# Kernel optimization log

Hardware: AMD Instinct MI355X
Metric: run time of the kernel (lower is better)

The kernel has to match this reference:

```python
import jax, jax.numpy as jnp
import numpy as np

HORIZON_K = 20
EPS = 1e-8


def _unfold_gather(x, time_idx, k):
    # Emulates zero-pad + tensor.unfold(1, k, 1).permute(3,0,1,2) + index_select(2, time_idx)
    # x: [N, T-1, C] -> [k, N, S, C] where out[ki, n, s] = x_padded[n, time_idx[s] + ki]
    N, Tm1, C = x.shape
    xp = jnp.concatenate([x, jnp.zeros((N, k, C), x.dtype)], axis=1)
    gidx = time_idx[None, :] + jnp.arange(k)[:, None]  # [k, S]
    return jnp.transpose(xp[:, gidx, :], (1, 0, 2, 3))  # [k, N, S, C]


def _gru_rollout(x_seq, h0, W_ih, W_hh, b_ih, b_hh):
    # x_seq: [k, B, A]; h0: [B, H]; torch GRU gate order: r, z, n
    H = h0.shape[-1]
    def step(h, x):
        gi = x @ W_ih.T + b_ih          # [B, 3H]
        gh = h @ W_hh.T + b_hh          # [B, 3H]
        r = jax.nn.sigmoid(gi[:, :H] + gh[:, :H])
        z = jax.nn.sigmoid(gi[:, H:2 * H] + gh[:, H:2 * H])
        n = jnp.tanh(gi[:, 2 * H:] + r * gh[:, 2 * H:])
        hn = (1.0 - z) * n + z * h
        return hn, hn
    _, hs = jax.lax.scan(step, h0, x_seq)
    return hs  # [k, B, H]


def _mlp(x, W1, b1, W2, b2, W3, b3):
    x = jax.nn.relu(x @ W1 + b1)
    x = jax.nn.relu(x @ W2 + b2)
    return x @ W3 + b3


def _l2norm(x):
    n = jnp.linalg.norm(x, axis=-1, keepdims=True)
    return x / jnp.maximum(n, EPS)


def setup_inputs() -> dict:
    key = jax.random.key(0)
    ks = jax.random.split(key, 16)
    N, T, H, A, M = 1024, 128, 256, 18, 512
    g = lambda k, sh, s: jax.random.normal(k, sh, jnp.float32) * s
    return {
        "actions": jax.random.randint(ks[0], (N, T), 0, A),
        "dones": jnp.zeros((N, T), jnp.float32),
        "b_t": g(ks[1], (N * T, H), 1.0),
        "z_t": g(ks[2], (N * T, H), 1.0),
        "time_subsample": jax.random.randint(ks[3], (6,), 0, T - 1),
        "unroll_subsample": jax.random.randint(ks[4], (2,), 0, HORIZON_K),
        "W_ih": g(ks[5], (3 * H, A), 0.05), "W_hh": g(ks[6], (3 * H, H), 0.05),
        "b_ih": g(ks[7], (3 * H,), 0.05), "b_hh": g(ks[8], (3 * H,), 0.05),
        "W1": g(ks[9], (H, M), 0.05), "b1": g(ks[10], (M,), 0.05),
        "W2": g(ks[11], (M, M), 0.05), "b2": g(ks[12], (M,), 0.05),
        "W3": g(ks[13], (M, H), 0.05), "b3": g(ks[14], (H,), 0.05),
    }


def reference(actions, dones, b_t, z_t, time_subsample, unroll_subsample,
              W_ih, W_hh, b_ih, b_hh, W1, b1, W2, b2, W3, b3):
    N, T = actions.shape
    H = b_t.shape[-1]
    A = W_ih.shape[1]
    k = HORIZON_K

    # mask (dones fixed to all-zero -> max_k == horizon_k)
    not_dones = (1.0 - dones).reshape(N, T, 1)
    nd_unf = _unfold_gather(not_dones[:, :-1], time_subsample, k)        # [k,N,S,1]
    fmask = jnp.cumprod(nd_unf, axis=0).reshape(k, -1, 1)                # [k,N*S,1]
    fmask = (fmask[unroll_subsample] > 0).astype(jnp.float32)            # [F,B,1]

    # unfolded one-hot actions
    onehot = jax.nn.one_hot(actions, A, dtype=jnp.float32)               # [N,T,A]
    act_unf = _unfold_gather(onehot[:, :-1], time_subsample, k)          # [k,N,S,A]
    act_unf = act_unf.reshape(k, -1, A)                                  # [k,B,A]

    # GRU initial states from core outputs at subsampled times
    c = b_t.reshape(N, T, H)[:, :-1][:, time_subsample]                  # [N,S,H]
    h0 = c.reshape(-1, H)                                                # [B,H]

    # 20-step open-loop GRU rollout
    h_pred = _gru_rollout(act_unf, h0, W_ih, W_hh, b_ih, b_hh)           # [k,B,H]
    h_pred = h_pred[unroll_subsample]                                    # [F,B,H]

    final_pred = _mlp(h_pred, W1, b1, W2, b2, W3, b3)                    # [F,B,H]
    norm = jnp.linalg.norm(final_pred, axis=2)
    reg = 0.02 * jnp.square(norm - 1.0)                                  # [F,B]
    final_pred = _l2norm(final_pred)

    # targets (no grad): unfolded future encodings, normalized
    z = jax.lax.stop_gradient(z_t).reshape(N, T, -1)
    tgt = _unfold_gather(z[:, 1:], time_subsample, k)                    # [k,N,S,C]
    tgt = tgt[unroll_subsample].reshape(len(unroll_subsample), -1, z.shape[-1])
    tgt = _l2norm(tgt)                                                   # [F,B,C]

    loss = jnp.square(final_pred - tgt)                                  # [F,B,C]
    loss = loss.mean(-1, keepdims=True)                                  # [F,B,1]
    loss = jnp.sum(loss * fmask) / jnp.maximum(jnp.sum(fmask), 1.0)
    return loss + reg.mean()
```

## Files before the change

### kernel.cpp

```cpp
#include <hip/hip_runtime.h>
#include <hip/hip_bf16.h>
#include <math.h>

#define NN 1024
#define TT 128
#define SS 6
#define FF 2
#define HH 256
#define AA 18
#define MM 512
#define KH 20
#define BB (NN*SS)
#define RR (FF*BB)
#define LOSS_BLOCKS 1024

#define SCL_RZ (-1.44269504089f)
#define SCL_N  (-2.88539008178f)
#define TBL_STRIDE 784

typedef __bf16 bf16x8 __attribute__((ext_vector_type(8)));
typedef float f32x4 __attribute__((ext_vector_type(4)));

__device__ __forceinline__ f32x4 mfma16(bf16x8 a, bf16x8 b, f32x4 c) {
    return __builtin_amdgcn_mfma_f32_16x16x32_bf16(a, b, c, 0, 0, 0);
}
__device__ __forceinline__ unsigned short f2b(float f) {
    return __builtin_bit_cast(unsigned short, __float2bfloat16(f));
}
__device__ __forceinline__ float rcp_f(float x)  { return __builtin_amdgcn_rcpf(x); }
__device__ __forceinline__ float exp2_f(float x) { return __builtin_amdgcn_exp2f(x); }

#define OFF_ACT   0UL
#define OFF_HPRED 491520UL
#define OFF_PRED  6782976UL
#define OFF_WHH   19365888UL
#define OFF_W1T   19759104UL
#define OFF_W2T   20021248UL
#define OFF_W3T   20545536UL
#define OFF_TBL   20807680UL
#define OFF_PART  20867264UL

__global__ void k_prep(const float* __restrict__ Whh, const float* __restrict__ W1,
                       const float* __restrict__ W2, const float* __restrict__ W3,
                       const float* __restrict__ Wih, const float* __restrict__ bih,
                       const float* __restrict__ bhh,
                       const int* __restrict__ actions, const int* __restrict__ ts,
                       unsigned short* whh_s, unsigned short* w1t, unsigned short* w2t,
                       unsigned short* w3t, float* tbl, int* act) {
    int idx = blockIdx.x * 256 + threadIdx.x;
    if (idx < 196608) {
        int wrow = idx >> 8;
        float scl = (wrow < 512) ? SCL_RZ : SCL_N;
        whh_s[idx] = f2b(Whh[idx] * scl);
        return;
    }
    idx -= 196608;
    if (idx < 131072) { int m = idx >> 8, k = idx & 255; w1t[idx] = f2b(W1[k * MM + m]); return; }
    idx -= 131072;
    if (idx < 262144) { int m = idx >> 9, k = idx & 511; w2t[idx] = f2b(W2[k * MM + m]); return; }
    idx -= 262144;
    if (idx < 131072) { int c = idx >> 9, k = idx & 511; w3t[idx] = f2b(W3[k * HH + c]); return; }
    idx -= 131072;
    if (idx < 19 * TBL_STRIDE) {
        int a = idx / TBL_STRIDE, rem = idx - a * TBL_STRIDE;
        float v = 0.f;
        if (rem < 768) {
            int g = rem >> 8;
            float scl = (g < 2) ? SCL_RZ : SCL_N;
            float w = (a < AA) ? Wih[rem * AA + a] : 0.f;
            v = scl * (w + bih[rem] + ((g < 2) ? bhh[rem] : 0.f));
        }
        tbl[idx] = v;
        return;
    }
    idx -= 19 * TBL_STRIDE;
    {
        int b = idx / KH, k = idx - b * KH;
        int n = b / SS, s = b - n * SS;
        int tt = ts[s] + k;
        act[idx] = (tt < TT - 1) ? actions[n * TT + tt] : AA;
    }
}

__global__ void __launch_bounds__(512, 2)
k_gru_all(const unsigned short* __restrict__ whh_s, const float* __restrict__ tblg,
          const float* __restrict__ bhh, const int* __restrict__ actg,
          const int* __restrict__ us, const int* __restrict__ ts,
          const float* __restrict__ b_t, unsigned short* __restrict__ hpred) {
    __shared__ float tbl[19 * TBL_STRIDE];
    __shared__ int act_l[16][KH];
    __shared__ unsigned short htile[16][264];

    int tid = threadIdx.x, wave = tid >> 6, lane = tid & 63;
    int l15 = lane & 15, grp = lane >> 4, lk8 = grp << 3, r4 = grp << 2;
    int rb = blockIdx.x * 16;
    int u0 = us[0], u1 = us[1];
    int kmax = u0 > u1 ? u0 : u1;

    for (int i = tid; i < 19 * TBL_STRIDE / 4; i += 512)
        reinterpret_cast<float4*>(tbl)[i] = reinterpret_cast<const float4*>(tblg)[i];
    if (tid < 16 * KH) {
        int r = tid / KH, k = tid - r * KH;
        act_l[r][k] = actg[(rb + r) * KH + k];
    }

    bf16x8 wr[6][8];
#pragma unroll
    for (int ct = 0; ct < 6; ++ct) {
        int wrow = (ct >> 1) * 256 + wave * 32 + (ct & 1) * 16 + l15;
        const unsigned short* base = &whh_s[(size_t)wrow * HH];
#pragma unroll
        for (int kk = 0; kk < 8; ++kk)
            wr[ct][kk] = *reinterpret_cast<const bf16x8*>(&base[kk * 32 + lk8]);
    }

    float hm[2][4];
#pragma unroll
    for (int cj = 0; cj < 2; ++cj)
#pragma unroll
        for (int reg = 0; reg < 4; ++reg) {
            int b = rb + r4 + reg;
            int n = b / SS, s = b - n * SS;
            hm[cj][reg] = b_t[(size_t)(n * TT + ts[s]) * HH + wave * 32 + cj * 16 + l15];
        }
    float bhn[2];
#pragma unroll
    for (int cj = 0; cj < 2; ++cj) bhn[cj] = SCL_N * bhh[512 + wave * 32 + cj * 16 + l15];

    {
        int row = tid >> 5, c8 = (tid & 31) << 3;
        int b = rb + row;
        int n = b / SS, s = b - n * SS;
        const float* src = &b_t[(size_t)(n * TT + ts[s]) * HH + c8];
        uint4 pk;
        pk.x = f2b(src[0]) | ((unsigned)f2b(src[1]) << 16);
        pk.y = f2b(src[2]) | ((unsigned)f2b(src[3]) << 16);
        pk.z = f2b(src[4]) | ((unsigned)f2b(src[5]) << 16);
        pk.w = f2b(src[6]) | ((unsigned)f2b(src[7]) << 16);
        *reinterpret_cast<uint4*>(&htile[row][c8]) = pk;
    }
    __syncthreads();

    for (int ki = 0; ki <= kmax; ++ki) {
        f32x4 aR[2] = {}, aZ[2] = {}, aN[2] = {};
#pragma unroll
        for (int kk = 0; kk < 8; ++kk) {
            bf16x8 ah = *reinterpret_cast<const bf16x8*>(&htile[l15][kk * 32 + lk8]);
            aR[0] = mfma16(ah, wr[0][kk], aR[0]);
            aR[1] = mfma16(ah, wr[1][kk], aR[1]);
            aZ[0] = mfma16(ah, wr[2][kk], aZ[0]);
            aZ[1] = mfma16(ah, wr[3][kk], aZ[1]);
            aN[0] = mfma16(ah, wr[4][kk], aN[0]);
            aN[1] = mfma16(ah, wr[5][kk], aN[1]);
        }
        __syncthreads();

#pragma unroll
        for (int cj = 0; cj < 2; ++cj) {
            int j2 = wave * 32 + cj * 16 + l15;
            float bhnv = bhn[cj];
#pragma unroll
            for (int reg = 0; reg < 4; ++reg) {
                int row = r4 + reg;
                const float* tb = &tbl[act_l[row][ki] * TBL_STRIDE];
                float r = rcp_f(1.f + exp2_f(aR[cj][reg] + tb[j2]));
                float z = rcp_f(1.f + exp2_f(aZ[cj][reg] + tb[256 + j2]));
                float ghn = aN[cj][reg] + bhnv;
                float nv = 2.f * rcp_f(1.f + exp2_f(tb[512 + j2] + r * ghn)) - 1.f;
                float h = hm[cj][reg];
                float hn2 = nv + z * (h - nv);
                hm[cj][reg] = hn2;
                unsigned short hbv = f2b(hn2);
                htile[row][j2] = hbv;
                if (ki == u0) hpred[(size_t)(rb + row) * HH + j2] = hbv;
                if (ki == u1) hpred[(size_t)(BB + rb + row) * HH + j2] = hbv;
            }
        }
        __syncthreads();
    }
}

__device__ __forceinline__ int xsw(int row, int chunk) {
    return (row << 9) + ((chunk ^ (row & 7)) << 3);
}

__global__ void __launch_bounds__(512, 2)
k_mlp_all(const unsigned short* __restrict__ hpred, const unsigned short* __restrict__ w1t,
          const unsigned short* __restrict__ w2t, const unsigned short* __restrict__ w3t,
          const float* __restrict__ b1, const float* __restrict__ b2,
          const float* __restrict__ b3, float* __restrict__ pred) {
    __shared__ unsigned short xs[48 * 512];
    int tid = threadIdx.x, wave = tid >> 6, lane = tid & 63;
    int l15 = lane & 15, grp = lane >> 4, lk8 = grp << 3, r4 = grp << 2;
    int rb = blockIdx.x * 48;

    {
        f32x4 acc[3][4] = {};
        for (int kk = 0; kk < 8; ++kk) {
            int k0 = kk * 32 + lk8;
            bf16x8 av[3];
#pragma unroll
            for (int rt = 0; rt < 3; ++rt)
                av[rt] = *reinterpret_cast<const bf16x8*>(&hpred[(size_t)(rb + rt * 16 + l15) * HH + k0]);
#pragma unroll
            for (int ct = 0; ct < 4; ++ct) {
                int col = wave * 64 + ct * 16 + l15;
                bf16x8 bv = *reinterpret_cast<const bf16x8*>(&w1t[(size_t)col * HH + k0]);
#pragma unroll
                for (int rt = 0; rt < 3; ++rt) acc[rt][ct] = mfma16(av[rt], bv, acc[rt][ct]);
            }
        }
#pragma unroll
        for (int ct = 0; ct < 4; ++ct) {
            int col = wave * 64 + ct * 16 + l15;
            float bb = b1[col];
#pragma unroll
            for (int rt = 0; rt < 3; ++rt)
#pragma unroll
                for (int reg = 0; reg < 4; ++reg) {
                    int row = rt * 16 + r4 + reg;
                    xs[xsw(row, col >> 3) + (col & 7)] = f2b(fmaxf(acc[rt][ct][reg] + bb, 0.f));
                }
        }
    }
    __syncthreads();

    {
        f32x4 acc[3][4] = {};
        for (int kk = 0; kk < 16; ++kk) {
            bf16x8 av[3];
#pragma unroll
            for (int rt = 0; rt < 3; ++rt)
                av[rt] = *reinterpret_cast<const bf16x8*>(&xs[xsw(rt * 16 + l15, kk * 4 + grp)]);
#pragma unroll
            for (int ct = 0; ct < 4; ++ct) {
                int col = wave * 64 + ct * 16 + l15;
                bf16x8 bv = *reinterpret_cast<const bf16x8*>(&w2t[(size_t)col * MM + kk * 32 + lk8]);
#pragma unroll
                for (int rt = 0; rt < 3; ++rt) acc[rt][ct] = mfma16(av[rt], bv, acc[rt][ct]);
            }
        }
        __syncthreads();
#pragma unroll
        for (int ct = 0; ct < 4; ++ct) {
            int col = wave * 64 + ct * 16 + l15;
            float bb = b2[col];
#pragma unroll
            for (int rt = 0; rt < 3; ++rt)
#pragma unroll
                for (int reg = 0; reg < 4; ++reg) {
                    int row = rt * 16 + r4 + reg;
                    xs[xsw(row, col >> 3) + (col & 7)] = f2b(fmaxf(acc[rt][ct][reg] + bb, 0.f));
                }
        }
    }
    __syncthreads();

    {
        f32x4 acc[3][2] = {};
        for (int kk = 0; kk < 16; ++kk) {
            bf16x8 av[3];
#pragma unroll
            for (int rt = 0; rt < 3; ++rt)
                av[rt] = *reinterpret_cast<const bf16x8*>(&xs[xsw(rt * 16 + l15, kk * 4 + grp)]);
#pragma unroll
            for (int ct = 0; ct < 2; ++ct) {
                int col = wave * 32 + ct * 16 + l15;
                bf16x8 bv = *reinterpret_cast<const bf16x8*>(&w3t[(size_t)col * MM + kk * 32 + lk8]);
#pragma unroll
                for (int rt = 0; rt < 3; ++rt) acc[rt][ct] = mfma16(av[rt], bv, acc[rt][ct]);
            }
        }
#pragma unroll
        for (int ct = 0; ct < 2; ++ct) {
            int col = wave * 32 + ct * 16 + l15;
            float bb = b3[col];
#pragma unroll
            for (int rt = 0; rt < 3; ++rt)
#pragma unroll
                for (int reg = 0; reg < 4; ++reg) {
                    int row = rt * 16 + r4 + reg;
                    pred[(size_t)(rb + row) * HH + col] = acc[rt][ct][reg] + bb;
                }
        }
    }
}

__global__ void k_loss(const float* __restrict__ pred, const float* __restrict__ z_t,
                       const float* __restrict__ dones, const int* __restrict__ ts,
                       const int* __restrict__ us, float* part) {
    int wave = threadIdx.x >> 6, lane = threadIdx.x & 63;
    float mse_l = 0.f;
    float cnt_l = 0.f, reg_l = 0.f;

    for (int i = 0; i < 3; ++i) {
        int row = blockIdx.x * 12 + wave * 3 + i;
        int f = row / BB, b = row - f * BB;
        int n = b / SS, s = b - n * SS;
        int t = ts[s], u = us[f];

        const float* pr = pred + (size_t)row * HH;
        float pv[4], ssq = 0.f;
#pragma unroll
        for (int q = 0; q < 4; ++q) { pv[q] = pr[lane + 64 * q]; ssq += pv[q] * pv[q]; }
        for (int o = 32; o; o >>= 1) ssq += __shfl_xor(ssq, o);
        float norm = sqrtf(ssq);
        if (lane == 0) { float d = norm - 1.f; reg_l += 0.02f * d * d; }

        bool valid = (t + u) < (TT - 1);
        if (valid) {
            float m = 1.f;
            for (int jj = 0; jj <= u; ++jj) m *= (1.f - dones[n * TT + t + jj]);
            valid = (m > 0.f);
        }
        if (!valid) continue;

        const float* zr = z_t + (size_t)(n * TT + 1 + t + u) * HH;
        float zv[4], zsq = 0.f;
#pragma unroll
        for (int q = 0; q < 4; ++q) { zv[q] = zr[lane + 64 * q]; zsq += zv[q] * zv[q]; }
        for (int o = 32; o; o >>= 1) zsq += __shfl_xor(zsq, o);
        float tn = sqrtf(zsq);

        float ip = 1.f / fmaxf(norm, 1e-8f);
        float it = 1.f / fmaxf(tn, 1e-8f);
        float e = 0.f;
#pragma unroll
        for (int q = 0; q < 4; ++q) { float d = pv[q] * ip - zv[q] * it; e += d * d; }
        mse_l += e * (1.f / HH);
        if (lane == 0) cnt_l += 1.f;
    }

    for (int o = 32; o; o >>= 1) mse_l += __shfl_xor(mse_l, o);

    __shared__ float sm[4][3];
    if (lane == 0) { sm[wave][0] = mse_l; sm[wave][1] = cnt_l; sm[wave][2] = reg_l; }
    __syncthreads();
    if (threadIdx.x == 0) {
        float s0 = 0.f, s1 = 0.f, s2 = 0.f;
        for (int w = 0; w < 4; ++w) { s0 += sm[w][0]; s1 += sm[w][1]; s2 += sm[w][2]; }
        part[blockIdx.x * 3 + 0] = s0;
        part[blockIdx.x * 3 + 1] = s1;
        part[blockIdx.x * 3 + 2] = s2;
    }
}

__global__ void k_final(const float* __restrict__ part, float* out) {
    int tid = threadIdx.x, wave = tid >> 6, lane = tid & 63;
    float s0 = 0.f, s1 = 0.f, s2 = 0.f;
    for (int i = tid; i < LOSS_BLOCKS; i += 256) {
        s0 += part[i * 3 + 0];
        s1 += part[i * 3 + 1];
        s2 += part[i * 3 + 2];
    }
    for (int o = 32; o; o >>= 1) {
        s0 += __shfl_xor(s0, o);
        s1 += __shfl_xor(s1, o);
        s2 += __shfl_xor(s2, o);
    }
    __shared__ float sm[4][3];
    if (lane == 0) { sm[wave][0] = s0; sm[wave][1] = s1; sm[wave][2] = s2; }
    __syncthreads();
    if (tid == 0) {
        float a = 0.f, b = 0.f, c = 0.f;
        for (int w = 0; w < 4; ++w) { a += sm[w][0]; b += sm[w][1]; c += sm[w][2]; }
        out[0] = a / fmaxf(b, 1.f) + c * (1.f / RR);
    }
}

extern "C" void kernel_launch(void* const* d_in, const int* in_sizes, int n_in,
                              void* d_out, int out_size, void* d_ws, size_t ws_size,
                              hipStream_t stream) {
    const int*   actions = (const int*)d_in[0];
    const float* dones   = (const float*)d_in[1];
    const float* b_t     = (const float*)d_in[2];
    const float* z_t     = (const float*)d_in[3];
    const int*   ts      = (const int*)d_in[4];
    const int*   us      = (const int*)d_in[5];
    const float* W_ih    = (const float*)d_in[6];
    const float* W_hh    = (const float*)d_in[7];
    const float* b_ih    = (const float*)d_in[8];
    const float* b_hh    = (const float*)d_in[9];
    const float* W1      = (const float*)d_in[10];
    const float* b1      = (const float*)d_in[11];
    const float* W2      = (const float*)d_in[12];
    const float* b2      = (const float*)d_in[13];
    const float* W3      = (const float*)d_in[14];
    const float* b3      = (const float*)d_in[15];

    char* ws = (char*)d_ws;
    int*            act   = (int*)(ws + OFF_ACT);
    unsigned short* hpred = (unsigned short*)(ws + OFF_HPRED);
    float*          pred  = (float*)(ws + OFF_PRED);
    unsigned short* whh_s = (unsigned short*)(ws + OFF_WHH);
    unsigned short* w1t   = (unsigned short*)(ws + OFF_W1T);
    unsigned short* w2t   = (unsigned short*)(ws + OFF_W2T);
    unsigned short* w3t   = (unsigned short*)(ws + OFF_W3T);
    float*          tbl   = (float*)(ws + OFF_TBL);
    float*          part  = (float*)(ws + OFF_PART);

    k_prep<<<3355, 256, 0, stream>>>(W_hh, W1, W2, W3, W_ih, b_ih, b_hh, actions, ts,
                                     whh_s, w1t, w2t, w3t, tbl, act);
    k_gru_all<<<384, 512, 0, stream>>>(whh_s, tbl, b_hh, act, us, ts, b_t, hpred);
    k_mlp_all<<<256, 512, 0, stream>>>(hpred, w1t, w2t, w3t, b1, b2, b3, pred);
    k_loss<<<LOSS_BLOCKS, 256, 0, stream>>>(pred, z_t, dones, ts, us, part);
    k_final<<<1, 256, 0, stream>>>(part, (float*)d_out);
}
```

Baseline: 114.0 us.

## Fuse loss into MLP kernel and batch 24 rows per GRU block

The loss computation moves into the MLP kernel's epilogue. Per-row norms and dot products are computed from the MLP output and a bf16 copy of the target staged in shared memory, so the fp32 prediction buffer and the separate loss kernel are no longer needed. The GRU kernel now handles 24 rows per block across 256 blocks and double-buffers the hidden-state tile, which removes one barrier per step. The previous hidden state is read back from the bf16 tile instead of fp32 registers, and the target is rounded to bf16, so accuracy drops slightly. Launch bounds on the MLP kernel also rise to 4 blocks per CU.

Result: no change. 115.1 us (+0.9%).

```diff
diff --git a/kernel.cpp b/kernel.cpp
--- a/kernel.cpp
+++ b/kernel.cpp
@@ -12,7 +12,6 @@
 #define KH 20
 #define BB (NN*SS)
 #define RR (FF*BB)
-#define LOSS_BLOCKS 1024
 
 #define SCL_RZ (-1.44269504089f)
 #define SCL_N  (-2.88539008178f)
@@ -27,18 +26,20 @@
 __device__ __forceinline__ unsigned short f2b(float f) {
     return __builtin_bit_cast(unsigned short, __float2bfloat16(f));
 }
+__device__ __forceinline__ float b2f(unsigned short u) {
+    return __builtin_bit_cast(float, (unsigned)u << 16);
+}
 __device__ __forceinline__ float rcp_f(float x)  { return __builtin_amdgcn_rcpf(x); }
 __device__ __forceinline__ float exp2_f(float x) { return __builtin_amdgcn_exp2f(x); }
 
 #define OFF_ACT   0UL
 #define OFF_HPRED 491520UL
-#define OFF_PRED  6782976UL
-#define OFF_WHH   19365888UL
-#define OFF_W1T   19759104UL
-#define OFF_W2T   20021248UL
-#define OFF_W3T   20545536UL
-#define OFF_TBL   20807680UL
-#define OFF_PART  20867264UL
+#define OFF_WHH   6782976UL
+#define OFF_W1T   7176192UL
+#define OFF_W2T   7438336UL
+#define OFF_W3T   7962624UL
+#define OFF_TBL   8224768UL
+#define OFF_PART  8284352UL
 
 __global__ void k_prep(const float* __restrict__ Whh, const float* __restrict__ W1,
                        const float* __restrict__ W2, const float* __restrict__ W3,
@@ -74,7 +75,7 @@
         return;
     }
     idx -= 19 * TBL_STRIDE;
-    {
+    if (idx < BB * KH) {
         int b = idx / KH, k = idx - b * KH;
         int n = b / SS, s = b - n * SS;
         int tt = ts[s] + k;
@@ -88,20 +89,35 @@
           const int* __restrict__ us, const int* __restrict__ ts,
           const float* __restrict__ b_t, unsigned short* __restrict__ hpred) {
     __shared__ float tbl[19 * TBL_STRIDE];
-    __shared__ int act_l[16][KH];
-    __shared__ unsigned short htile[16][264];
+    __shared__ unsigned short htile[2][32][264];
+    __shared__ int act_l[24][KH];
 
     int tid = threadIdx.x, wave = tid >> 6, lane = tid & 63;
     int l15 = lane & 15, grp = lane >> 4, lk8 = grp << 3, r4 = grp << 2;
-    int rb = blockIdx.x * 16;
+    int rb = blockIdx.x * 24;
     int u0 = us[0], u1 = us[1];
     int kmax = u0 > u1 ? u0 : u1;
 
     for (int i = tid; i < 19 * TBL_STRIDE / 4; i += 512)
         reinterpret_cast<float4*>(tbl)[i] = reinterpret_cast<const float4*>(tblg)[i];
-    if (tid < 16 * KH) {
-        int r = tid / KH, k = tid - r * KH;
-        act_l[r][k] = actg[(rb + r) * KH + k];
+    if (tid < 24 * KH) {
+        int r = tid / KH, k2 = tid - r * KH;
+        act_l[r][k2] = actg[(rb + r) * KH + k2];
+    }
+
+    for (int i = tid; i < 2 * 32 * 32; i += 512) {
+        int buf = i >> 10, rem = i & 1023, row = rem >> 5, c8 = (rem & 31) << 3;
+        uint4 pk = {0u, 0u, 0u, 0u};
+        if (buf == 0 && row < 24) {
+            int b = rb + row;
+            int n = b / SS, s = b - n * SS;
+            const float* src = &b_t[(size_t)(n * TT + ts[s]) * HH + c8];
+            pk.x = f2b(src[0]) | ((unsigned)f2b(src[1]) << 16);
+            pk.y = f2b(src[2]) | ((unsigned)f2b(src[3]) << 16);
+            pk.z = f2b(src[4]) | ((unsigned)f2b(src[5]) << 16);
+            pk.w = f2b(src[6]) | ((unsigned)f2b(src[7]) << 16);
+        }
+        *reinterpret_cast<uint4*>(&htile[buf][row][c8]) = pk;
     }
 
     bf16x8 wr[6][8];
@@ -113,70 +129,52 @@
         for (int kk = 0; kk < 8; ++kk)
             wr[ct][kk] = *reinterpret_cast<const bf16x8*>(&base[kk * 32 + lk8]);
     }
-
-    float hm[2][4];
-#pragma unroll
-    for (int cj = 0; cj < 2; ++cj)
-#pragma unroll
-        for (int reg = 0; reg < 4; ++reg) {
-            int b = rb + r4 + reg;
-            int n = b / SS, s = b - n * SS;
-            hm[cj][reg] = b_t[(size_t)(n * TT + ts[s]) * HH + wave * 32 + cj * 16 + l15];
-        }
     float bhn[2];
 #pragma unroll
     for (int cj = 0; cj < 2; ++cj) bhn[cj] = SCL_N * bhh[512 + wave * 32 + cj * 16 + l15];
-
-    {
-        int row = tid >> 5, c8 = (tid & 31) << 3;
-        int b = rb + row;
-        int n = b / SS, s = b - n * SS;
-        const float* src = &b_t[(size_t)(n * TT + ts[s]) * HH + c8];
-        uint4 pk;
-        pk.x = f2b(src[0]) | ((unsigned)f2b(src[1]) << 16);
-        pk.y = f2b(src[2]) | ((unsigned)f2b(src[3]) << 16);
-        pk.z = f2b(src[4]) | ((unsigned)f2b(src[5]) << 16);
-        pk.w = f2b(src[6]) | ((unsigned)f2b(src[7]) << 16);
-        *reinterpret_cast<uint4*>(&htile[row][c8]) = pk;
-    }
     __syncthreads();
 
+    int cur = 0;
     for (int ki = 0; ki <= kmax; ++ki) {
-        f32x4 aR[2] = {}, aZ[2] = {}, aN[2] = {};
-#pragma unroll
-        for (int kk = 0; kk < 8; ++kk) {
-            bf16x8 ah = *reinterpret_cast<const bf16x8*>(&htile[l15][kk * 32 + lk8]);
-            aR[0] = mfma16(ah, wr[0][kk], aR[0]);
-            aR[1] = mfma16(ah, wr[1][kk], aR[1]);
-            aZ[0] = mfma16(ah, wr[2][kk], aZ[0]);
-            aZ[1] = mfma16(ah, wr[3][kk], aZ[1]);
-            aN[0] = mfma16(ah, wr[4][kk], aN[0]);
-            aN[1] = mfma16(ah, wr[5][kk], aN[1]);
+        int nxt = cur ^ 1;
+#pragma unroll
+        for (int rt = 0; rt < 2; ++rt) {
+            f32x4 aR[2] = {}, aZ[2] = {}, aN[2] = {};
+#pragma unroll
+            for (int kk = 0; kk < 8; ++kk) {
+                bf16x8 ah = *reinterpret_cast<const bf16x8*>(&htile[cur][rt * 16 + l15][kk * 32 + lk8]);
+                aR[0] = mfma16(ah, wr[0][kk], aR[0]);
+                aR[1] = mfma16(ah, wr[1][kk], aR[1]);
+                aZ[0] = mfma16(ah, wr[2][kk], aZ[0]);
+                aZ[1] = mfma16(ah, wr[3][kk], aZ[1]);
+                aN[0] = mfma16(ah, wr[4][kk], aN[0]);
+                aN[1] = mfma16(ah, wr[5][kk], aN[1]);
+            }
+#pragma unroll
+            for (int cj = 0; cj < 2; ++cj) {
+                int j2 = wave * 32 + cj * 16 + l15;
+                float bhnv = bhn[cj];
+#pragma unroll
+                for (int reg = 0; reg < 4; ++reg) {
+                    int rowl = rt * 16 + r4 + reg;
+                    if (rt == 0 || rowl < 24) {
+                        const float* tb = &tbl[act_l[rowl][ki] * TBL_STRIDE];
+                        float r = rcp_f(1.f + exp2_f(aR[cj][reg] + tb[j2]));
+                        float z = rcp_f(1.f + exp2_f(aZ[cj][reg] + tb[256 + j2]));
+                        float ghn = aN[cj][reg] + bhnv;
+                        float nv = 2.f * rcp_f(1.f + exp2_f(tb[512 + j2] + r * ghn)) - 1.f;
+                        float h = b2f(htile[cur][rowl][j2]);
+                        float hn2 = nv + z * (h - nv);
+                        unsigned short hbv = f2b(hn2);
+                        htile[nxt][rowl][j2] = hbv;
+                        if (ki == u0) hpred[(size_t)(rb + rowl) * HH + j2] = hbv;
+                        if (ki == u1) hpred[(size_t)(BB + rb + rowl) * HH + j2] = hbv;
+                    }
+                }
+            }
         }
         __syncthreads();
-
-#pragma unroll
-        for (int cj = 0; cj < 2; ++cj) {
-            int j2 = wave * 32 + cj * 16 + l15;
-            float bhnv = bhn[cj];
-#pragma unroll
-            for (int reg = 0; reg < 4; ++reg) {
-                int row = r4 + reg;
-                const float* tb = &tbl[act_l[row][ki] * TBL_STRIDE];
-                float r = rcp_f(1.f + exp2_f(aR[cj][reg] + tb[j2]));
-                float z = rcp_f(1.f + exp2_f(aZ[cj][reg] + tb[256 + j2]));
-                float ghn = aN[cj][reg] + bhnv;
-                float nv = 2.f * rcp_f(1.f + exp2_f(tb[512 + j2] + r * ghn)) - 1.f;
-                float h = hm[cj][reg];
-                float hn2 = nv + z * (h - nv);
-                hm[cj][reg] = hn2;
-                unsigned short hbv = f2b(hn2);
-                htile[row][j2] = hbv;
-                if (ki == u0) hpred[(size_t)(rb + row) * HH + j2] = hbv;
-                if (ki == u1) hpred[(size_t)(BB + rb + row) * HH + j2] = hbv;
-            }
-        }
-        __syncthreads();
+        cur = nxt;
     }
 }
 
@@ -184,15 +182,47 @@
     return (row << 9) + ((chunk ^ (row & 7)) << 3);
 }
 
-__global__ void __launch_bounds__(512, 2)
-k_mlp_all(const unsigned short* __restrict__ hpred, const unsigned short* __restrict__ w1t,
-          const unsigned short* __restrict__ w2t, const unsigned short* __restrict__ w3t,
-          const float* __restrict__ b1, const float* __restrict__ b2,
-          const float* __restrict__ b3, float* __restrict__ pred) {
+__global__ void __launch_bounds__(512, 4)
+k_mlp_loss(const unsigned short* __restrict__ hpred, const unsigned short* __restrict__ w1t,
+           const unsigned short* __restrict__ w2t, const unsigned short* __restrict__ w3t,
+           const float* __restrict__ b1, const float* __restrict__ b2,
+           const float* __restrict__ b3, const float* __restrict__ z_t,
+           const float* __restrict__ dones, const int* __restrict__ ts,
+           const int* __restrict__ us, float* __restrict__ part) {
     __shared__ unsigned short xs[48 * 512];
+    __shared__ unsigned short zs[48 * 256];
+    __shared__ float rstat[48][8][3];
+    __shared__ float vmask[48];
+
     int tid = threadIdx.x, wave = tid >> 6, lane = tid & 63;
     int l15 = lane & 15, grp = lane >> 4, lk8 = grp << 3, r4 = grp << 2;
     int rb = blockIdx.x * 48;
+
+    if (tid < 48) {
+        int rg = rb + tid;
+        int f = rg >= BB ? 1 : 0;
+        int b = rg - f * BB;
+        int n = b / SS, s = b - n * SS;
+        int t = ts[s], u = us[f];
+        float m = (t + u < TT - 1) ? 1.f : 0.f;
+        if (m > 0.f) for (int j = 0; j <= u; ++j) m *= (1.f - dones[n * TT + t + j]);
+        vmask[tid] = (m > 0.f) ? 1.f : 0.f;
+    }
+    for (int i = tid; i < 48 * 64; i += 512) {
+        int row = i >> 6, c4 = (i & 63) << 2;
+        int rg = rb + row;
+        int f = rg >= BB ? 1 : 0;
+        int b = rg - f * BB;
+        int n = b / SS, s = b - n * SS;
+        int t = ts[s], u = us[f];
+        uint2 pk = {0u, 0u};
+        if (t + u < TT - 1) {
+            float4 v = *reinterpret_cast<const float4*>(&z_t[(size_t)(n * TT + 1 + t + u) * HH + c4]);
+            pk.x = f2b(v.x) | ((unsigned)f2b(v.y) << 16);
+            pk.y = f2b(v.z) | ((unsigned)f2b(v.w) << 16);
+        }
+        *reinterpret_cast<uint2*>(&zs[row * 256 + c4]) = pk;
+    }
 
     {
         f32x4 acc[3][4] = {};
@@ -217,10 +247,9 @@
 #pragma unroll
             for (int rt = 0; rt < 3; ++rt)
 #pragma unroll
-                for (int reg = 0; reg < 4; ++reg) {
-                    int row = rt * 16 + r4 + reg;
-                    xs[xsw(row, col >> 3) + (col & 7)] = f2b(fmaxf(acc[rt][ct][reg] + bb, 0.f));
-                }
+                for (int reg = 0; reg < 4; ++reg)
+                    xs[xsw(rt * 16 + r4 + reg, col >> 3) + (col & 7)] =
+                        f2b(fmaxf(acc[rt][ct][reg] + bb, 0.f));
         }
     }
     __syncthreads();
@@ -248,10 +277,9 @@
 #pragma unroll
             for (int rt = 0; rt < 3; ++rt)
 #pragma unroll
-                for (int reg = 0; reg < 4; ++reg) {
-                    int row = rt * 16 + r4 + reg;
-                    xs[xsw(row, col >> 3) + (col & 7)] = f2b(fmaxf(acc[rt][ct][reg] + bb, 0.f));
-                }
+                for (int reg = 0; reg < 4; ++reg)
+                    xs[xsw(rt * 16 + r4 + reg, col >> 3) + (col & 7)] =
+                        f2b(fmaxf(acc[rt][ct][reg] + bb, 0.f));
         }
     }
     __syncthreads();
@@ -271,84 +299,72 @@
                 for (int rt = 0; rt < 3; ++rt) acc[rt][ct] = mfma16(av[rt], bv, acc[rt][ct]);
             }
         }
-#pragma unroll
-        for (int ct = 0; ct < 2; ++ct) {
-            int col = wave * 32 + ct * 16 + l15;
-            float bb = b3[col];
-#pragma unroll
-            for (int rt = 0; rt < 3; ++rt)
-#pragma unroll
-                for (int reg = 0; reg < 4; ++reg) {
-                    int row = rt * 16 + r4 + reg;
-                    pred[(size_t)(rb + row) * HH + col] = acc[rt][ct][reg] + bb;
+        float b3c0 = b3[wave * 32 + l15];
+        float b3c1 = b3[wave * 32 + 16 + l15];
+#pragma unroll
+        for (int rt = 0; rt < 3; ++rt)
+#pragma unroll
+            for (int reg = 0; reg < 4; ++reg) {
+                int row = rt * 16 + r4 + reg;
+                float p0 = acc[rt][0][reg] + b3c0;
+                float p1 = acc[rt][1][reg] + b3c1;
+                float z0 = b2f(zs[row * 256 + wave * 32 + l15]);
+                float z1 = b2f(zs[row * 256 + wave * 32 + 16 + l15]);
+                float psq = p0 * p0 + p1 * p1;
+                float zsq = z0 * z0 + z1 * z1;
+                float pz  = p0 * z0 + p1 * z1;
+#pragma unroll
+                for (int o = 1; o < 16; o <<= 1) {
+                    psq += __shfl_xor(psq, o);
+                    zsq += __shfl_xor(zsq, o);
+                    pz  += __shfl_xor(pz, o);
                 }
-        }
-    }
-}
-
-__global__ void k_loss(const float* __restrict__ pred, const float* __restrict__ z_t,
-                       const float* __restrict__ dones, const int* __restrict__ ts,
-                       const int* __restrict__ us, float* part) {
-    int wave = threadIdx.x >> 6, lane = threadIdx.x & 63;
-    float mse_l = 0.f;
-    float cnt_l = 0.f, reg_l = 0.f;
-
-    for (int i = 0; i < 3; ++i) {
-        int row = blockIdx.x * 12 + wave * 3 + i;
-        int f = row / BB, b = row - f * BB;
-        int n = b / SS, s = b - n * SS;
-        int t = ts[s], u = us[f];
-
-        const float* pr = pred + (size_t)row * HH;
-        float pv[4], ssq = 0.f;
-#pragma unroll
-        for (int q = 0; q < 4; ++q) { pv[q] = pr[lane + 64 * q]; ssq += pv[q] * pv[q]; }
-        for (int o = 32; o; o >>= 1) ssq += __shfl_xor(ssq, o);
-        float norm = sqrtf(ssq);
-        if (lane == 0) { float d = norm - 1.f; reg_l += 0.02f * d * d; }
-
-        bool valid = (t + u) < (TT - 1);
-        if (valid) {
-            float m = 1.f;
-            for (int jj = 0; jj <= u; ++jj) m *= (1.f - dones[n * TT + t + jj]);
-            valid = (m > 0.f);
-        }
-        if (!valid) continue;
-
-        const float* zr = z_t + (size_t)(n * TT + 1 + t + u) * HH;
-        float zv[4], zsq = 0.f;
-#pragma unroll
-        for (int q = 0; q < 4; ++q) { zv[q] = zr[lane + 64 * q]; zsq += zv[q] * zv[q]; }
-        for (int o = 32; o; o >>= 1) zsq += __shfl_xor(zsq, o);
-        float tn = sqrtf(zsq);
-
-        float ip = 1.f / fmaxf(norm, 1e-8f);
-        float it = 1.f / fmaxf(tn, 1e-8f);
-        float e = 0.f;
-#pragma unroll
-        for (int q = 0; q < 4; ++q) { float d = pv[q] * ip - zv[q] * it; e += d * d; }
-        mse_l += e * (1.f / HH);
-        if (lane == 0) cnt_l += 1.f;
-    }
-
-    for (int o = 32; o; o >>= 1) mse_l += __shfl_xor(mse_l, o);
-
-    __shared__ float sm[4][3];
-    if (lane == 0) { sm[wave][0] = mse_l; sm[wave][1] = cnt_l; sm[wave][2] = reg_l; }
+                if (l15 == 0) {
+                    rstat[row][wave][0] = psq;
+                    rstat[row][wave][1] = zsq;
+                    rstat[row][wave][2] = pz;
+                }
+            }
+    }
     __syncthreads();
-    if (threadIdx.x == 0) {
-        float s0 = 0.f, s1 = 0.f, s2 = 0.f;
-        for (int w = 0; w < 4; ++w) { s0 += sm[w][0]; s1 += sm[w][1]; s2 += sm[w][2]; }
-        part[blockIdx.x * 3 + 0] = s0;
-        part[blockIdx.x * 3 + 1] = s1;
-        part[blockIdx.x * 3 + 2] = s2;
+
+    if (tid < 64) {
+        float a0 = 0.f, a1 = 0.f, a2 = 0.f;
+        if (tid < 48) {
+            float sp = 0.f, sz = 0.f, spz = 0.f;
+#pragma unroll
+            for (int w = 0; w < 8; ++w) {
+                sp  += rstat[tid][w][0];
+                sz  += rstat[tid][w][1];
+                spz += rstat[tid][w][2];
+            }
+            float npn = sqrtf(sp), nzn = sqrtf(sz);
+            float d = npn - 1.f;
+            a2 = 0.02f * d * d;
+            float mp = fmaxf(npn, 1e-8f), mz = fmaxf(nzn, 1e-8f);
+            float lossr = (sp / (mp * mp) + sz / (mz * mz) - 2.f * spz / (mp * mz)) * (1.f / HH);
+            float vm = vmask[tid];
+            a0 = vm * lossr;
+            a1 = vm;
+        }
+#pragma unroll
+        for (int o = 1; o < 64; o <<= 1) {
+            a0 += __shfl_xor(a0, o);
+            a1 += __shfl_xor(a1, o);
+            a2 += __shfl_xor(a2, o);
+        }
+        if (tid == 0) {
+            part[blockIdx.x * 3 + 0] = a0;
+            part[blockIdx.x * 3 + 1] = a1;
+            part[blockIdx.x * 3 + 2] = a2;
+        }
     }
 }
 
 __global__ void k_final(const float* __restrict__ part, float* out) {
     int tid = threadIdx.x, wave = tid >> 6, lane = tid & 63;
     float s0 = 0.f, s1 = 0.f, s2 = 0.f;
-    for (int i = tid; i < LOSS_BLOCKS; i += 256) {
+    for (int i = tid; i < 256; i += 256) {
         s0 += part[i * 3 + 0];
         s1 += part[i * 3 + 1];
         s2 += part[i * 3 + 2];
@@ -391,7 +407,6 @@
     char* ws = (char*)d_ws;
     int*            act   = (int*)(ws + OFF_ACT);
     unsigned short* hpred = (unsigned short*)(ws + OFF_HPRED);
-    float*          pred  = (float*)(ws + OFF_PRED);
     unsigned short* whh_s = (unsigned short*)(ws + OFF_WHH);
     unsigned short* w1t   = (unsigned short*)(ws + OFF_W1T);
     unsigned short* w2t   = (unsigned short*)(ws + OFF_W2T);
@@ -401,8 +416,8 @@
 
     k_prep<<<3355, 256, 0, stream>>>(W_hh, W1, W2, W3, W_ih, b_ih, b_hh, actions, ts,
                                      whh_s, w1t, w2t, w3t, tbl, act);
-    k_gru_all<<<384, 512, 0, stream>>>(whh_s, tbl, b_hh, act, us, ts, b_t, hpred);
-    k_mlp_all<<<256, 512, 0, stream>>>(hpred, w1t, w2t, w3t, b1, b2, b3, pred);
-    k_loss<<<LOSS_BLOCKS, 256, 0, stream>>>(pred, z_t, dones, ts, us, part);
+    k_gru_all<<<256, 512, 0, stream>>>(whh_s, tbl, b_hh, act, us, ts, b_t, hpred);
+    k_mlp_loss<<<256, 512, 0, stream>>>(hpred, w1t, w2t, w3t, b1, b2, b3,
+                                        z_t, dones, ts, us, part);
     k_final<<<1, 256, 0, stream>>>(part, (float*)d_out);
 }
```
